# Kernel tuning notes

Hardware: AMD Instinct MI355X
Metric: run time of the kernel (lower is better)

The kernel has to match this reference:

```python
import jax, jax.numpy as jnp
import numpy as np

H, D_MODEL = 12, 768
D_K = D_MODEL // H
B, S = 2, 2048


def setup_inputs() -> dict:
    key = jax.random.key(0)
    ks = jax.random.split(key, 11)
    sc = 0.02
    return {
        "query": jax.random.normal(ks[0], (B, S, D_MODEL), jnp.float32),
        "key": jax.random.normal(ks[1], (B, S, D_MODEL), jnp.float32),
        "value": jax.random.normal(ks[2], (B, S, D_MODEL), jnp.float32),
        # per-head Linear weights, torch layout [out, in] -> stacked [h, d_k, d_model]
        "Wq": jax.random.normal(ks[3], (H, D_K, D_MODEL), jnp.float32) * sc,
        "bq": jax.random.normal(ks[4], (H, D_K), jnp.float32) * sc,
        "Wk": jax.random.normal(ks[5], (H, D_K, D_MODEL), jnp.float32) * sc,
        "bk": jax.random.normal(ks[6], (H, D_K), jnp.float32) * sc,
        "Wv": jax.random.normal(ks[7], (H, D_K, D_MODEL), jnp.float32) * sc,
        "bv": jax.random.normal(ks[8], (H, D_K), jnp.float32) * sc,
        "Wo": jax.random.normal(ks[9], (D_MODEL, D_MODEL), jnp.float32) * sc,
        "bo": jax.random.normal(ks[10], (D_MODEL,), jnp.float32) * sc,
    }


def reference(query, key, value, Wq, bq, Wk, bk, Wv, bv, Wo, bo):
    # per-head projections: [B,S,D] x [H,Dk,D] -> [B,H,S,Dk]
    q = jnp.einsum("bsd,hkd->bhsk", query, Wq) + bq[None, :, None, :]
    k = jnp.einsum("bsd,hkd->bhsk", key, Wk) + bk[None, :, None, :]
    v = jnp.einsum("bsd,hkd->bhsk", value, Wv) + bv[None, :, None, :]
    # scaled dot-product attention (full [B,H,S,S] scores, as in the original)
    scores = jnp.einsum("bhqk,bhsk->bhqs", q, k) * (1.0 / jnp.sqrt(jnp.asarray(D_K, q.dtype)))
    attn = jax.nn.softmax(scores, axis=-1)
    ctx = jnp.einsum("bhqs,bhsk->bhqk", attn, v)
    # merge heads: [B,H,S,Dk] -> [B,S,H*Dk]
    ctx = ctx.transpose(0, 2, 1, 3).reshape(query.shape[0], -1, H * D_K)
    # output projection (torch Linear: x @ W.T + b)
    return ctx @ Wo.T + bo
```

## Files before the change

kernel.cpp:

```cpp
#include <hip/hip_runtime.h>
#include <math.h>
#include <stdint.h>

#define H_  12
#define DK_ 64
#define DM_ 768
#define B_  2
#define S_  2048

typedef __bf16 bf16x8 __attribute__((ext_vector_type(8)));
typedef __bf16 bf16x4_t __attribute__((ext_vector_type(4)));
typedef float  f32x4  __attribute__((ext_vector_type(4)));

__device__ __forceinline__ void gload16(const void* gsrc, void* ldst) {
    using GPtr = const __attribute__((address_space(1))) void*;
    using LPtr = __attribute__((address_space(3))) void*;
    __builtin_amdgcn_global_load_lds((GPtr)(uintptr_t)gsrc, (LPtr)(uintptr_t)ldst, 16, 0, 0);
}

__device__ __forceinline__ void bar() {
    asm volatile("" ::: "memory");
    __builtin_amdgcn_s_barrier();
    asm volatile("" ::: "memory");
}
__device__ __forceinline__ void bar_end() {
    asm volatile("s_waitcnt lgkmcnt(0)" ::: "memory");
    __builtin_amdgcn_s_barrier();
    asm volatile("" ::: "memory");
}
#define WAITVM(N) asm volatile("s_waitcnt vmcnt(" #N ")" ::: "memory")

template<int OFF>
__device__ __forceinline__ bf16x8 trread8(uint32_t addr) {
    union { bf16x8 v; bf16x4_t h[2]; } u;
    asm volatile("ds_read_b64_tr_b16 %0, %2 offset:%3\n\t"
                 "ds_read_b64_tr_b16 %1, %2 offset:%4"
                 : "=v"(u.h[0]), "=v"(u.h[1])
                 : "v"(addr), "i"(OFF), "i"(OFF + 128));
    return u.v;
}

__global__ __launch_bounds__(256)
void prep(const float* __restrict__ q, const float* __restrict__ k,
          const float* __restrict__ v,
          const float* __restrict__ wq, const float* __restrict__ wk,
          const float* __restrict__ wv, const float* __restrict__ wo,
          __bf16* __restrict__ qo, __bf16* __restrict__ ko, __bf16* __restrict__ vo,
          __bf16* __restrict__ wqh, __bf16* __restrict__ wkh,
          __bf16* __restrict__ wvh, __bf16* __restrict__ woh,
          __bf16* __restrict__ wol)
{
    const int NIN = 786432;
    int gid = blockIdx.x * 256 + threadIdx.x;
    if (gid < 3 * NIN) {
        int which = gid / NIN, i = gid - which * NIN;
        const float* src = which == 0 ? q : (which == 1 ? k : v);
        __bf16* dst = which == 0 ? qo : (which == 1 ? ko : vo);
        float4 a = ((const float4*)src)[i];
        bf16x4_t h;
        h[0]=(__bf16)a.x; h[1]=(__bf16)a.y; h[2]=(__bf16)a.z; h[3]=(__bf16)a.w;
        *(bf16x4_t*)&dst[i*4] = h;
    } else {
        int i = gid - 3 * NIN;
        float4 a; bf16x4_t h, l;
        a = ((const float4*)wq)[i];
        h[0]=(__bf16)a.x; h[1]=(__bf16)a.y; h[2]=(__bf16)a.z; h[3]=(__bf16)a.w;
        *(bf16x4_t*)&wqh[i*4] = h;
        a = ((const float4*)wk)[i];
        h[0]=(__bf16)a.x; h[1]=(__bf16)a.y; h[2]=(__bf16)a.z; h[3]=(__bf16)a.w;
        *(bf16x4_t*)&wkh[i*4] = h;
        a = ((const float4*)wv)[i];
        h[0]=(__bf16)a.x; h[1]=(__bf16)a.y; h[2]=(__bf16)a.z; h[3]=(__bf16)a.w;
        *(bf16x4_t*)&wvh[i*4] = h;
        a = ((const float4*)wo)[i];
        h[0]=(__bf16)a.x; h[1]=(__bf16)a.y; h[2]=(__bf16)a.z; h[3]=(__bf16)a.w;
        l[0]=(__bf16)(a.x-(float)h[0]); l[1]=(__bf16)(a.y-(float)h[1]);
        l[2]=(__bf16)(a.z-(float)h[2]); l[3]=(__bf16)(a.w-(float)h[3]);
        *(bf16x4_t*)&woh[i*4] = h;
        *(bf16x4_t*)&wol[i*4] = l;
    }
}

__global__ __launch_bounds__(256)
void proj_gemm(const __bf16* __restrict__ x0, const __bf16* __restrict__ x1,
               const __bf16* __restrict__ x2,
               const __bf16* __restrict__ w0, const __bf16* __restrict__ w1,
               const __bf16* __restrict__ w2,
               const float* __restrict__ b0, const float* __restrict__ b1,
               const float* __restrict__ b2,
               __bf16* __restrict__ o0, __bf16* __restrict__ o1,
               __bf16* __restrict__ o2,
               float s0, float s1, float s2)
{
    __shared__ __align__(16) __bf16 sA[2][64 * 64];
    __shared__ __align__(16) __bf16 sW[2][128 * 64];

    const int tid = threadIdx.x;
    const int w = tid >> 6, lane = tid & 63;
    const int g = lane >> 4, c16 = lane & 15;
    const int wr = w >> 1, wc = w & 1;

    const int z = blockIdx.z;
    const __bf16* A  = z == 0 ? x0 : (z == 1 ? x1 : x2);
    const __bf16* W  = z == 0 ? w0 : (z == 1 ? w1 : w2);
    const float* bias = z == 0 ? b0 : (z == 1 ? b1 : b2);
    __bf16* out = z == 0 ? o0 : (z == 1 ? o1 : o2);
    const float scale = z == 0 ? s0 : (z == 1 ? s1 : s2);

    int flat = blockIdx.y * 6 + blockIdx.x;
    int swz  = (flat & 7) * 48 + (flat >> 3);
    int nx = swz % 6, my = swz / 6;
    const int m0 = my * 64, n0 = nx * 128;

    const int rj  = tid >> 3;
    const int rsw = ((tid & 7) ^ (rj & 7)) << 3;
    const __bf16* asrc = A + (size_t)(m0 + rj) * 768 + rsw;
    const __bf16* wsrc = W + (size_t)(n0 + rj) * 768 + rsw;

    f32x4 acc[2][4] = {};

    auto STAGE = [&](int kk, int buf) {
        #pragma unroll
        for (int i = 0; i < 2; ++i)
            gload16(asrc + (size_t)(i * 32) * 768 + kk,
                    (char*)&sA[buf][0] + (i * 256 + tid) * 16);
        #pragma unroll
        for (int i = 0; i < 4; ++i)
            gload16(wsrc + (size_t)(i * 32) * 768 + kk,
                    (char*)&sW[buf][0] + (i * 256 + tid) * 16);
    };

    STAGE(0, 0);
    int cur = 0;
    for (int k0 = 0; k0 < 768; k0 += 64) {
        if (k0 + 64 < 768) { STAGE(k0 + 64, cur ^ 1); WAITVM(6); }
        else               { WAITVM(0); }
        bar();
        const __bf16* Ab = &sA[cur][0];
        const __bf16* Wb = &sW[cur][0];
        #pragma unroll
        for (int ks = 0; ks < 2; ++ks) {
            bf16x8 ah[2];
            #pragma unroll
            for (int rt = 0; rt < 2; ++rt) {
                int j = wr * 32 + rt * 16 + c16;
                ah[rt] = *(const bf16x8*)&Ab[j * 64 + ((((ks << 2) | g) ^ (j & 7)) << 3)];
            }
            __builtin_amdgcn_s_setprio(1);
            #pragma unroll
            for (int ct = 0; ct < 4; ++ct) {
                int j = wc * 64 + ct * 16 + c16;
                bf16x8 bh = *(const bf16x8*)&Wb[j * 64 + ((((ks << 2) | g) ^ (j & 7)) << 3)];
                #pragma unroll
                for (int rt = 0; rt < 2; ++rt)
                    acc[rt][ct] = __builtin_amdgcn_mfma_f32_16x16x32_bf16(ah[rt], bh, acc[rt][ct], 0, 0, 0);
            }
            __builtin_amdgcn_s_setprio(0);
        }
        bar_end();
        cur ^= 1;
    }

    #pragma unroll
    for (int rt = 0; rt < 2; ++rt)
        #pragma unroll
        for (int ct = 0; ct < 4; ++ct) {
            int n = n0 + wc * 64 + ct * 16 + c16;
            float bv = bias[n];
            #pragma unroll
            for (int e = 0; e < 4; ++e) {
                int m = m0 + wr * 32 + rt * 16 + g * 4 + e;
                float val = (acc[rt][ct][e] + bv) * scale;
                int b = m >> 11, s = m & (S_ - 1);
                int h = n >> 6,  dk = n & 63;
                out[(((size_t)b * H_ + h) * S_ + s) * DK_ + dk] = (__bf16)val;
            }
        }
}

__global__ __launch_bounds__(256)
void out_gemm(const __bf16* __restrict__ Ah, const __bf16* __restrict__ Al,
              const __bf16* __restrict__ Wh, const __bf16* __restrict__ Wl,
              const float* __restrict__ bias, float* __restrict__ out)
{
    __shared__ __align__(16) __bf16 sAh[2][64*64], sAl[2][64*64];
    __shared__ __align__(16) __bf16 sWh[2][64*64], sWl[2][64*64];

    const int tid = threadIdx.x;
    const int w = tid >> 6, lane = tid & 63;
    const int g = lane >> 4, c16 = lane & 15;
    const int wr = w >> 1, wc = w & 1;

    int flat = blockIdx.y * 12 + blockIdx.x;
    int swz  = (flat & 7) * 96 + (flat >> 3);
    int nx = swz % 12, my = swz / 12;
    const int m0 = my * 64, n0 = nx * 64;

    const int rj  = tid >> 3;
    const int rsw = ((tid & 7) ^ (rj & 7)) << 3;
    const __bf16* ahs = Ah + (size_t)(m0 + rj) * 768 + rsw;
    const __bf16* als = Al + (size_t)(m0 + rj) * 768 + rsw;
    const __bf16* whs = Wh + (size_t)(n0 + rj) * 768 + rsw;
    const __bf16* wls = Wl + (size_t)(n0 + rj) * 768 + rsw;

    f32x4 acc[2][2] = {};

    auto STAGE = [&](int kk, int buf) {
        #pragma unroll
        for (int i = 0; i < 2; ++i) {
            size_t so = (size_t)(i * 32) * 768 + kk;
            int dof = (i * 256 + tid) * 16;
            gload16(ahs + so, (char*)&sAh[buf][0] + dof);
            gload16(als + so, (char*)&sAl[buf][0] + dof);
            gload16(whs + so, (char*)&sWh[buf][0] + dof);
            gload16(wls + so, (char*)&sWl[buf][0] + dof);
        }
    };

    STAGE(0, 0);
    int cur = 0;
    for (int k0 = 0; k0 < 768; k0 += 64) {
        if (k0 + 64 < 768) { STAGE(k0 + 64, cur ^ 1); WAITVM(8); }
        else               { WAITVM(0); }
        bar();
        #pragma unroll
        for (int ks = 0; ks < 2; ++ks) {
            bf16x8 va[2], la[2];
            #pragma unroll
            for (int rt = 0; rt < 2; ++rt) {
                int j = wr * 32 + rt * 16 + c16;
                int off = j * 64 + ((((ks << 2) | g) ^ (j & 7)) << 3);
                va[rt] = *(const bf16x8*)&sAh[cur][off];
                la[rt] = *(const bf16x8*)&sAl[cur][off];
            }
            __builtin_amdgcn_s_setprio(1);
            #pragma unroll
            for (int ct = 0; ct < 2; ++ct) {
                int j = wc * 32 + ct * 16 + c16;
                int off = j * 64 + ((((ks << 2) | g) ^ (j & 7)) << 3);
                bf16x8 bh = *(const bf16x8*)&sWh[cur][off];
                bf16x8 bl = *(const bf16x8*)&sWl[cur][off];
                #pragma unroll
                for (int rt = 0; rt < 2; ++rt) {
                    acc[rt][ct] = __builtin_amdgcn_mfma_f32_16x16x32_bf16(va[rt], bh, acc[rt][ct], 0, 0, 0);
                    acc[rt][ct] = __builtin_amdgcn_mfma_f32_16x16x32_bf16(la[rt], bh, acc[rt][ct], 0, 0, 0);
                    acc[rt][ct] = __builtin_amdgcn_mfma_f32_16x16x32_bf16(va[rt], bl, acc[rt][ct], 0, 0, 0);
                }
            }
            __builtin_amdgcn_s_setprio(0);
        }
        bar_end();
        cur ^= 1;
    }

    #pragma unroll
    for (int rt = 0; rt < 2; ++rt)
        #pragma unroll
        for (int ct = 0; ct < 2; ++ct) {
            int n = n0 + wc * 32 + ct * 16 + c16;
            float bv = bias[n];
            #pragma unroll
            for (int e = 0; e < 4; ++e) {
                int m = m0 + wr * 32 + rt * 16 + g * 4 + e;
                out[(size_t)m * 768 + n] = acc[rt][ct][e] + bv;
            }
        }
}

__global__ __launch_bounds__(256)
void attn_mfma(const __bf16* __restrict__ q, const __bf16* __restrict__ k,
               const __bf16* __restrict__ v,
               __bf16* __restrict__ ch, __bf16* __restrict__ cl)
{
    __shared__ __align__(16) __bf16 Ksm[2][64 * 64];
    __shared__ __align__(16) __bf16 Vsm[2][64 * 64];
    __shared__ __align__(16) __bf16 Psm[4][16 * 64];

    const int tid  = threadIdx.x;
    const int w    = tid >> 6;
    const int lane = tid & 63;
    const int g    = lane >> 4;
    const int c16  = lane & 15;

    int swzb = (blockIdx.x & 7) * 96 + (blockIdx.x >> 3);
    const int bh = swzb >> 5;
    const int q0 = (swzb & 31) * 64 + w * 16;
    const size_t base = (size_t)bh * S_ * DK_;

    bf16x8 qa[2];
    {
        const __bf16* qrow = q + base + (size_t)(q0 + c16) * DK_ + g * 8;
        qa[0] = *(const bf16x8*)(qrow);
        qa[1] = *(const bf16x8*)(qrow + 32);
    }

    f32x4 oacc[4] = {};
    float lr = 0.f;
    char* Pw = (char*)&Psm[w][0];
    const int psw = (c16 & 7);

    const int kj   = tid >> 3;
    const int ksw  = ((tid & 7) ^ (kj & 7)) << 3;
    const __bf16* ksrc0 = k + base + (size_t)kj * 64 + ksw;
    const int vkey = (tid >> 1) & 63;
    const int vt0  = tid >> 7;
    const int vhf  = (tid & 1) << 3;
    const __bf16* vsrc0 = v + base + (size_t)vkey * 64 + vhf;

    auto STAGE = [&](int kb, int buf) {
        #pragma unroll
        for (int i = 0; i < 2; ++i)
            gload16(ksrc0 + (size_t)(kb + i * 32) * 64,
                    (char*)&Ksm[buf][0] + (i * 256 + tid) * 16);
        #pragma unroll
        for (int i = 0; i < 2; ++i)
            gload16(vsrc0 + (size_t)kb * 64 + (vt0 + 2 * i) * 16,
                    (char*)&Vsm[buf][0] + (i * 256 + tid) * 16);
    };

    STAGE(0, 0);
    int cur = 0;
    for (int kb = 0; kb < S_; kb += 64) {
        if (kb + 64 < S_) { STAGE(kb + 64, cur ^ 1); WAITVM(4); }
        else              { WAITVM(0); }
        bar();

        const __bf16* Kb = &Ksm[cur][0];
        f32x4 sacc[4];
        #pragma unroll
        for (int t = 0; t < 4; ++t) {
            int krow = t * 16 + c16;
            f32x4 s_ = {};
            #pragma unroll
            for (int s = 0; s < 2; ++s) {
                bf16x8 kf = *(const bf16x8*)&Kb[krow * 64 + ((((s << 2) | g) ^ (krow & 7)) << 3)];
                s_ = __builtin_amdgcn_mfma_f32_16x16x32_bf16(kf, qa[s], s_, 0, 0, 0);
            }
            sacc[t] = s_;
        }

        uint32_t va = (uint32_t)(uintptr_t)&Vsm[cur][g * 128 + 4 * c16];
        bf16x8 tv0 = trread8<0>(va);
        bf16x8 tv1 = trread8<2048>(va);
        bf16x8 tv2 = trread8<4096>(va);
        bf16x8 tv3 = trread8<6144>(va);
        bf16x8 tv4 = trread8<1024>(va);
        bf16x8 tv5 = trread8<3072>(va);
        bf16x8 tv6 = trread8<5120>(va);
        bf16x8 tv7 = trread8<7168>(va);

        float csum = 0.f;
        #pragma unroll
        for (int t = 0; t < 4; ++t) {
            float p0 = exp2f(sacc[t][0]);
            float p1 = exp2f(sacc[t][1]);
            float p2 = exp2f(sacc[t][2]);
            float p3 = exp2f(sacc[t][3]);
            csum += (p0 + p1) + (p2 + p3);
            bf16x4_t pk;
            pk[0] = (__bf16)p0; pk[1] = (__bf16)p1;
            pk[2] = (__bf16)p2; pk[3] = (__bf16)p3;
            int c = 2 * t + (g >> 1);
            *(bf16x4_t*)(Pw + c16 * 128 + ((c ^ psw) << 4) + (g & 1) * 8) = pk;
        }
        lr += csum;

        bf16x8 pa0 = *(const bf16x8*)(Pw + c16 * 128 + ((g ^ psw) << 4));
        bf16x8 pa1 = *(const bf16x8*)(Pw + c16 * 128 + (((4 | g) ^ psw) << 4));
        asm volatile("s_waitcnt lgkmcnt(0)" ::: "memory");
        __builtin_amdgcn_sched_barrier(0);
        __builtin_amdgcn_s_setprio(1);
        oacc[0] = __builtin_amdgcn_mfma_f32_16x16x32_bf16(pa0, tv0, oacc[0], 0, 0, 0);
        oacc[1] = __builtin_amdgcn_mfma_f32_16x16x32_bf16(pa0, tv1, oacc[1], 0, 0, 0);
        oacc[2] = __builtin_amdgcn_mfma_f32_16x16x32_bf16(pa0, tv2, oacc[2], 0, 0, 0);
        oacc[3] = __builtin_amdgcn_mfma_f32_16x16x32_bf16(pa0, tv3, oacc[3], 0, 0, 0);
        oacc[0] = __builtin_amdgcn_mfma_f32_16x16x32_bf16(pa1, tv4, oacc[0], 0, 0, 0);
        oacc[1] = __builtin_amdgcn_mfma_f32_16x16x32_bf16(pa1, tv5, oacc[1], 0, 0, 0);
        oacc[2] = __builtin_amdgcn_mfma_f32_16x16x32_bf16(pa1, tv6, oacc[2], 0, 0, 0);
        oacc[3] = __builtin_amdgcn_mfma_f32_16x16x32_bf16(pa1, tv7, oacc[3], 0, 0, 0);
        __builtin_amdgcn_s_setprio(0);

        bar_end();
        cur ^= 1;
    }

    lr += __shfl_xor(lr, 16, 64);
    lr += __shfl_xor(lr, 32, 64);

    int b = bh / H_, h = bh % H_;
    #pragma unroll
    for (int r = 0; r < 4; ++r) {
        int srcl = (lane & 48) | (g * 4 + r);
        float lsum = __shfl(lr, srcl, 64);
        float inv = 1.0f / lsum;
        int row = q0 + g * 4 + r;
        size_t o = ((size_t)b * S_ + row) * DM_ + h * DK_ + c16;
        #pragma unroll
        for (int t = 0; t < 4; ++t) {
            float val = oacc[t][r] * inv;
            __bf16 hi = (__bf16)val;
            ch[o + t * 16] = hi;
            cl[o + t * 16] = (__bf16)(val - (float)hi);
        }
    }
}

extern "C" void kernel_launch(void* const* d_in, const int* in_sizes, int n_in,
                              void* d_out, int out_size, void* d_ws, size_t ws_size,
                              hipStream_t stream)
{
    const float* query = (const float*)d_in[0];
    const float* key   = (const float*)d_in[1];
    const float* value = (const float*)d_in[2];
    const float* Wq    = (const float*)d_in[3];
    const float* bq    = (const float*)d_in[4];
    const float* Wk    = (const float*)d_in[5];
    const float* bk    = (const float*)d_in[6];
    const float* Wv    = (const float*)d_in[7];
    const float* bv    = (const float*)d_in[8];
    const float* Wo    = (const float*)d_in[9];
    const float* bo    = (const float*)d_in[10];
    float* out = (float*)d_out;

    const size_t TSZ = (size_t)B_ * S_ * DM_;
    const size_t WSZ = (size_t)DM_ * DM_;
    __bf16* p  = (__bf16*)d_ws;
    __bf16* xq = p;
    __bf16* xk = xq + TSZ;
    __bf16* xv = xk + TSZ;
    __bf16* qh = xv + TSZ;
    __bf16* kh = qh + TSZ;
    __bf16* vh = kh + TSZ;
    __bf16* wqh = vh + TSZ;
    __bf16* wkh = wqh + WSZ;
    __bf16* wvh = wkh + WSZ;
    __bf16* woh = wvh + WSZ;
    __bf16* wol = woh + WSZ;
    __bf16* chh = xq;
    __bf16* cll = xk;

    prep<<<9792, 256, 0, stream>>>(query, key, value, Wq, Wk, Wv, Wo,
                                   xq, xk, xv, wqh, wkh, wvh, woh, wol);

    dim3 gp(6, 64, 3);
    proj_gemm<<<gp, 256, 0, stream>>>(xq, xk, xv, wqh, wkh, wvh,
                                      bq, bk, bv, qh, kh, vh,
                                      0.18033688011112f, 1.0f, 1.0f);

    attn_mfma<<<768, 256, 0, stream>>>(qh, kh, vh, chh, cll);

    dim3 go(12, 64);
    out_gemm<<<go, 256, 0, stream>>>(chh, cll, woh, wol, bo, out);
}
```

Before: 108.4 us.

## Split attention KV loop across wave pairs with 32-row query tiles per wave

Each wave now owns 32 query rows instead of 16, and pairs of waves split the key blocks by parity, so each wave processes every other 64-key tile. This reuses each K fragment and V transpose-read across two query tiles, halving LDS reads per MFMA. Partial outputs and row sums from the odd wave are merged through shared memory at the end. The costs are more accumulator registers, an extra barrier and reduction, and one wave of each pair idle on alternate iterations while still waiting at the barriers.

```diff
diff --git a/kernel.cpp b/kernel.cpp
--- a/kernel.cpp
+++ b/kernel.cpp
@@ -274,29 +274,33 @@
 {
     __shared__ __align__(16) __bf16 Ksm[2][64 * 64];
     __shared__ __align__(16) __bf16 Vsm[2][64 * 64];
-    __shared__ __align__(16) __bf16 Psm[4][16 * 64];
+    __shared__ __align__(16) __bf16 Psm[2][2][16 * 64];
 
     const int tid  = threadIdx.x;
     const int w    = tid >> 6;
     const int lane = tid & 63;
     const int g    = lane >> 4;
     const int c16  = lane & 15;
+    const int qp   = w >> 1;
+    const int par  = w & 1;
 
     int swzb = (blockIdx.x & 7) * 96 + (blockIdx.x >> 3);
     const int bh = swzb >> 5;
-    const int q0 = (swzb & 31) * 64 + w * 16;
+    const int q0 = (swzb & 31) * 64 + qp * 32;
     const size_t base = (size_t)bh * S_ * DK_;
 
-    bf16x8 qa[2];
-    {
-        const __bf16* qrow = q + base + (size_t)(q0 + c16) * DK_ + g * 8;
-        qa[0] = *(const bf16x8*)(qrow);
-        qa[1] = *(const bf16x8*)(qrow + 32);
-    }
-
-    f32x4 oacc[4] = {};
-    float lr = 0.f;
-    char* Pw = (char*)&Psm[w][0];
+    bf16x8 qa[2][2];
+    #pragma unroll
+    for (int qt = 0; qt < 2; ++qt) {
+        const __bf16* qrow = q + base + (size_t)(q0 + qt * 16 + c16) * DK_ + g * 8;
+        qa[qt][0] = *(const bf16x8*)(qrow);
+        qa[qt][1] = *(const bf16x8*)(qrow + 32);
+    }
+
+    f32x4 oacc[2][4] = {};
+    float lr0 = 0.f, lr1 = 0.f;
+    char* Pw0 = (char*)&Psm[qp][0][0];
+    char* Pw1 = (char*)&Psm[qp][1][0];
     const int psw = (c16 & 7);
 
     const int kj   = tid >> 3;
@@ -325,82 +329,122 @@
         else              { WAITVM(0); }
         bar();
 
-        const __bf16* Kb = &Ksm[cur][0];
-        f32x4 sacc[4];
-        #pragma unroll
-        for (int t = 0; t < 4; ++t) {
-            int krow = t * 16 + c16;
-            f32x4 s_ = {};
-            #pragma unroll
-            for (int s = 0; s < 2; ++s) {
-                bf16x8 kf = *(const bf16x8*)&Kb[krow * 64 + ((((s << 2) | g) ^ (krow & 7)) << 3)];
-                s_ = __builtin_amdgcn_mfma_f32_16x16x32_bf16(kf, qa[s], s_, 0, 0, 0);
-            }
-            sacc[t] = s_;
-        }
-
-        uint32_t va = (uint32_t)(uintptr_t)&Vsm[cur][g * 128 + 4 * c16];
-        bf16x8 tv0 = trread8<0>(va);
-        bf16x8 tv1 = trread8<2048>(va);
-        bf16x8 tv2 = trread8<4096>(va);
-        bf16x8 tv3 = trread8<6144>(va);
-        bf16x8 tv4 = trread8<1024>(va);
-        bf16x8 tv5 = trread8<3072>(va);
-        bf16x8 tv6 = trread8<5120>(va);
-        bf16x8 tv7 = trread8<7168>(va);
-
-        float csum = 0.f;
-        #pragma unroll
-        for (int t = 0; t < 4; ++t) {
-            float p0 = exp2f(sacc[t][0]);
-            float p1 = exp2f(sacc[t][1]);
-            float p2 = exp2f(sacc[t][2]);
-            float p3 = exp2f(sacc[t][3]);
-            csum += (p0 + p1) + (p2 + p3);
-            bf16x4_t pk;
-            pk[0] = (__bf16)p0; pk[1] = (__bf16)p1;
-            pk[2] = (__bf16)p2; pk[3] = (__bf16)p3;
-            int c = 2 * t + (g >> 1);
-            *(bf16x4_t*)(Pw + c16 * 128 + ((c ^ psw) << 4) + (g & 1) * 8) = pk;
-        }
-        lr += csum;
-
-        bf16x8 pa0 = *(const bf16x8*)(Pw + c16 * 128 + ((g ^ psw) << 4));
-        bf16x8 pa1 = *(const bf16x8*)(Pw + c16 * 128 + (((4 | g) ^ psw) << 4));
-        asm volatile("s_waitcnt lgkmcnt(0)" ::: "memory");
-        __builtin_amdgcn_sched_barrier(0);
-        __builtin_amdgcn_s_setprio(1);
-        oacc[0] = __builtin_amdgcn_mfma_f32_16x16x32_bf16(pa0, tv0, oacc[0], 0, 0, 0);
-        oacc[1] = __builtin_amdgcn_mfma_f32_16x16x32_bf16(pa0, tv1, oacc[1], 0, 0, 0);
-        oacc[2] = __builtin_amdgcn_mfma_f32_16x16x32_bf16(pa0, tv2, oacc[2], 0, 0, 0);
-        oacc[3] = __builtin_amdgcn_mfma_f32_16x16x32_bf16(pa0, tv3, oacc[3], 0, 0, 0);
-        oacc[0] = __builtin_amdgcn_mfma_f32_16x16x32_bf16(pa1, tv4, oacc[0], 0, 0, 0);
-        oacc[1] = __builtin_amdgcn_mfma_f32_16x16x32_bf16(pa1, tv5, oacc[1], 0, 0, 0);
-        oacc[2] = __builtin_amdgcn_mfma_f32_16x16x32_bf16(pa1, tv6, oacc[2], 0, 0, 0);
-        oacc[3] = __builtin_amdgcn_mfma_f32_16x16x32_bf16(pa1, tv7, oacc[3], 0, 0, 0);
-        __builtin_amdgcn_s_setprio(0);
-
+        if (((kb >> 6) & 1) == par) {
+            const __bf16* Kb = &Ksm[cur][0];
+            f32x4 s0[4], s1[4];
+            #pragma unroll
+            for (int t = 0; t < 4; ++t) {
+                int krow = t * 16 + c16;
+                f32x4 a0 = {}, a1 = {};
+                #pragma unroll
+                for (int s = 0; s < 2; ++s) {
+                    bf16x8 kf = *(const bf16x8*)&Kb[krow * 64 + ((((s << 2) | g) ^ (krow & 7)) << 3)];
+                    a0 = __builtin_amdgcn_mfma_f32_16x16x32_bf16(kf, qa[0][s], a0, 0, 0, 0);
+                    a1 = __builtin_amdgcn_mfma_f32_16x16x32_bf16(kf, qa[1][s], a1, 0, 0, 0);
+                }
+                s0[t] = a0; s1[t] = a1;
+            }
+
+            float cs0 = 0.f, cs1 = 0.f;
+            #pragma unroll
+            for (int t = 0; t < 4; ++t) {
+                int c = 2 * t + (g >> 1);
+                int coff = ((c ^ psw) << 4) + (g & 1) * 8;
+                {
+                    float p0 = exp2f(s0[t][0]), p1 = exp2f(s0[t][1]);
+                    float p2 = exp2f(s0[t][2]), p3 = exp2f(s0[t][3]);
+                    cs0 += (p0 + p1) + (p2 + p3);
+                    bf16x4_t pk;
+                    pk[0] = (__bf16)p0; pk[1] = (__bf16)p1;
+                    pk[2] = (__bf16)p2; pk[3] = (__bf16)p3;
+                    *(bf16x4_t*)(Pw0 + c16 * 128 + coff) = pk;
+                }
+                {
+                    float p0 = exp2f(s1[t][0]), p1 = exp2f(s1[t][1]);
+                    float p2 = exp2f(s1[t][2]), p3 = exp2f(s1[t][3]);
+                    cs1 += (p0 + p1) + (p2 + p3);
+                    bf16x4_t pk;
+                    pk[0] = (__bf16)p0; pk[1] = (__bf16)p1;
+                    pk[2] = (__bf16)p2; pk[3] = (__bf16)p3;
+                    *(bf16x4_t*)(Pw1 + c16 * 128 + coff) = pk;
+                }
+            }
+            lr0 += cs0; lr1 += cs1;
+
+            uint32_t va = (uint32_t)(uintptr_t)&Vsm[cur][g * 128 + 4 * c16];
+            #pragma unroll
+            for (int ks = 0; ks < 2; ++ks) {
+                int po = (((ks << 2) | g) ^ psw) << 4;
+                bf16x8 pa0 = *(const bf16x8*)(Pw0 + c16 * 128 + po);
+                bf16x8 pa1 = *(const bf16x8*)(Pw1 + c16 * 128 + po);
+                bf16x8 v0, v1, v2, v3;
+                if (ks == 0) {
+                    v0 = trread8<0>(va);    v1 = trread8<2048>(va);
+                    v2 = trread8<4096>(va); v3 = trread8<6144>(va);
+                } else {
+                    v0 = trread8<1024>(va); v1 = trread8<3072>(va);
+                    v2 = trread8<5120>(va); v3 = trread8<7168>(va);
+                }
+                asm volatile("s_waitcnt lgkmcnt(0)" ::: "memory");
+                __builtin_amdgcn_sched_barrier(0);
+                __builtin_amdgcn_s_setprio(1);
+                oacc[0][0] = __builtin_amdgcn_mfma_f32_16x16x32_bf16(pa0, v0, oacc[0][0], 0, 0, 0);
+                oacc[1][0] = __builtin_amdgcn_mfma_f32_16x16x32_bf16(pa1, v0, oacc[1][0], 0, 0, 0);
+                oacc[0][1] = __builtin_amdgcn_mfma_f32_16x16x32_bf16(pa0, v1, oacc[0][1], 0, 0, 0);
+                oacc[1][1] = __builtin_amdgcn_mfma_f32_16x16x32_bf16(pa1, v1, oacc[1][1], 0, 0, 0);
+                oacc[0][2] = __builtin_amdgcn_mfma_f32_16x16x32_bf16(pa0, v2, oacc[0][2], 0, 0, 0);
+                oacc[1][2] = __builtin_amdgcn_mfma_f32_16x16x32_bf16(pa1, v2, oacc[1][2], 0, 0, 0);
+                oacc[0][3] = __builtin_amdgcn_mfma_f32_16x16x32_bf16(pa0, v3, oacc[0][3], 0, 0, 0);
+                oacc[1][3] = __builtin_amdgcn_mfma_f32_16x16x32_bf16(pa1, v3, oacc[1][3], 0, 0, 0);
+                __builtin_amdgcn_s_setprio(0);
+            }
+        }
         bar_end();
         cur ^= 1;
     }
 
-    lr += __shfl_xor(lr, 16, 64);
-    lr += __shfl_xor(lr, 32, 64);
-
-    int b = bh / H_, h = bh % H_;
-    #pragma unroll
-    for (int r = 0; r < 4; ++r) {
-        int srcl = (lane & 48) | (g * 4 + r);
-        float lsum = __shfl(lr, srcl, 64);
-        float inv = 1.0f / lsum;
-        int row = q0 + g * 4 + r;
-        size_t o = ((size_t)b * S_ + row) * DM_ + h * DK_ + c16;
-        #pragma unroll
-        for (int t = 0; t < 4; ++t) {
-            float val = oacc[t][r] * inv;
-            __bf16 hi = (__bf16)val;
-            ch[o + t * 16] = hi;
-            cl[o + t * 16] = (__bf16)(val - (float)hi);
+    lr0 += __shfl_xor(lr0, 16, 64);
+    lr0 += __shfl_xor(lr0, 32, 64);
+    lr1 += __shfl_xor(lr1, 16, 64);
+    lr1 += __shfl_xor(lr1, 32, 64);
+
+    float* OX = (float*)&Ksm[0][0];
+    float* LX = (float*)&Vsm[0][0];
+    if (par == 1) {
+        #pragma unroll
+        for (int qt = 0; qt < 2; ++qt)
+            #pragma unroll
+            for (int t = 0; t < 4; ++t)
+                *(f32x4*)&OX[qp * 2048 + qt * 1024 + t * 256 + lane * 4] = oacc[qt][t];
+        LX[qp * 32 + 0 * 16 + c16] = lr0;
+        LX[qp * 32 + 1 * 16 + c16] = lr1;
+    }
+    bar();
+    if (par == 0) {
+        int b = bh / H_, h = bh % H_;
+        #pragma unroll
+        for (int qt = 0; qt < 2; ++qt) {
+            float lfull = (qt == 0 ? lr0 : lr1) + LX[qp * 32 + qt * 16 + c16];
+            #pragma unroll
+            for (int t = 0; t < 4; ++t) {
+                f32x4 po = *(const f32x4*)&OX[qp * 2048 + qt * 1024 + t * 256 + lane * 4];
+                oacc[qt][t][0] += po[0]; oacc[qt][t][1] += po[1];
+                oacc[qt][t][2] += po[2]; oacc[qt][t][3] += po[3];
+            }
+            #pragma unroll
+            for (int r = 0; r < 4; ++r) {
+                float lsum = __shfl(lfull, (lane & 48) | (g * 4 + r), 64);
+                float inv = 1.0f / lsum;
+                int row = q0 + qt * 16 + g * 4 + r;
+                size_t o = ((size_t)b * S_ + row) * DM_ + h * DK_ + c16;
+                #pragma unroll
+                for (int t = 0; t < 4; ++t) {
+                    float val = oacc[qt][t][r] * inv;
+                    __bf16 hi = (__bf16)val;
+                    ch[o + t * 16] = hi;
+                    cl[o + t * 16] = (__bf16)(val - (float)hi);
+                }
+            }
         }
     }
 }
```

Measured after the change: 120.5 us. +11.2%, slower.
